# Kernel optimization log

Measured on AMD Instinct MI355X. Metric: run time of the kernel, lower is better.

## Reference

```python
import jax, jax.numpy as jnp
import numpy as np

D, S, L, W, H, V = 64, 64, 64, 300, 300, 50000
NEG = jnp.float32(-9999999.0)


def setup_inputs() -> dict:
    key = jax.random.key(0)
    ks = jax.random.split(key, 16)
    n = lambda k, shape, s=0.05: jax.random.normal(k, shape, dtype=jnp.float32) * s
    return {
        "word_indices": jax.random.randint(ks[0], (D, S, L), 0, V),
        "E": n(ks[1], (V, W), 0.1),
        "W_sent": n(ks[2], (H, W)), "b_sent": jnp.zeros((H,), jnp.float32),
        "W_par": n(ks[3], (H, H)), "b_par": jnp.zeros((H,), jnp.float32),
        "W_ch": n(ks[4], (H, H)), "b_ch": jnp.zeros((H,), jnp.float32),
        "w_root": n(ks[5], (H,)), "b_root": jnp.zeros((), jnp.float32),
        "root_embed": n(ks[6], (H,)),
        "W_r": n(ks[7], (H, 3 * H)), "b_r": jnp.zeros((H,), jnp.float32),
        "W_cls": n(ks[8], (2, H)), "b_cls": jnp.zeros((2,), jnp.float32),
    }


def reference(word_indices, E, W_sent, b_sent, W_par, b_par, W_ch, b_ch,
              w_root, b_root, root_embed, W_r, b_r, W_cls, b_cls):
    lrelu = lambda x: jax.nn.leaky_relu(x, 0.01)
    # Ragged pad+gather stage of the original, dense here (all lengths == L)
    word_embed = E[word_indices]                 # [D,S,L,W]
    # 0.5*(X[l-1] + reverse(reverse(X))[l-1]) == X[l-1]; LSTM outputs unused in source
    x_last = word_embed[:, :, -1, :]             # [D,S,W]
    enc = lrelu(x_last @ W_sent.T + b_sent)      # [D,S,H] sentence encodings
    # Pairwise parent-child edge scores (O(S^2) dots in the original loops)
    P = lrelu(enc @ W_par.T + b_par)             # [D,S,H]
    C = lrelu(enc @ W_ch.T + b_ch)               # [D,S,H]
    A = jnp.einsum('dih,djh->dij', P, C)         # [D,S,S]
    A = jnp.where(jnp.eye(S, dtype=bool)[None], NEG, A)
    A = jax.nn.softmax(A, axis=1)                # Softmax(dim=0) per doc: over parents i
    scores = enc @ w_root + b_root               # [D,S] root scores
    fri = jax.nn.softmax(scores, axis=1)         # Softmax(dim=0) over sentences
    # ri[i] = r_embeds([enc_i, sum_k A[k,i]*enc_k + fri_i*root, enc_i*sum_k A[i,k]])
    tmp = jnp.einsum('dki,dkh->dih', A, enc)     # [D,S,H]
    agg = tmp + fri[..., None] * root_embed      # [D,S,H]
    tmp3 = enc * A.sum(axis=2, keepdims=True)    # [D,S,H]
    ri = lrelu(jnp.concatenate([enc, agg, tmp3], axis=-1) @ W_r.T + b_r)  # [D,S,H]
    final = ri.mean(axis=1)                      # [D,H]
    out = final @ W_cls.T + b_cls                # [D,2]
    return out, A, fri
```

## Files before the change

kernel.cpp:

```cpp
#include <hip/hip_runtime.h>

#define NEG_INF (-9999999.0f)

typedef __attribute__((ext_vector_type(8))) short bf16x8;
typedef __attribute__((ext_vector_type(4))) float f32x4;
typedef unsigned short us;
typedef unsigned int u32;

#define MFMA16 __builtin_amdgcn_mfma_f32_16x16x32_bf16

__device__ __forceinline__ float b2f(us u) {
  union { unsigned int i; float f; } x; x.i = ((unsigned int)u) << 16; return x.f;
}
__device__ __forceinline__ us f2b(float f) {
  union { float f; unsigned int i; } x; x.f = f;
  unsigned int r = x.i + 0x7fffu + ((x.i >> 16) & 1u);
  return (us)(r >> 16);
}
__device__ __forceinline__ float lrelu(float v) { return v > 0.f ? v : 0.01f * v; }
__device__ __forceinline__ bf16x8 ld8(const us* p) { return *reinterpret_cast<const bf16x8*>(p); }
__device__ __forceinline__ int swz(int row) { return (row & 7) << 4; }

__global__ __launch_bounds__(256) void k_prep(
    const float* __restrict__ Ws, const float* __restrict__ Wp, const float* __restrict__ Wc,
    const float* __restrict__ Wr, const float* __restrict__ root,
    us* __restrict__ Wsb, us* __restrict__ Wpb, us* __restrict__ Wcb,
    us* __restrict__ Wr3b, float* __restrict__ c2) {
  int task = blockIdx.y;
  int gid = blockIdx.x * 256 + threadIdx.x;
  const int stride = 80 * 256;
  if (task < 3) {
    const float* src = (task == 0) ? Ws : (task == 1) ? Wp : Wc;
    us* dst = (task == 0) ? Wsb : (task == 1) ? Wpb : Wcb;
    for (int i = gid; i < 320 * 320; i += stride) {
      int r = i / 320, c = i - r * 320;
      dst[i] = (r < 300 && c < 300) ? f2b(src[r * 300 + c]) : (us)0;
    }
  } else if (task == 3) {
    for (int i = gid; i < 3 * 320 * 320; i += stride) {
      int seg = i / 102400, rem = i - seg * 102400;
      int r = rem / 320, c = rem - r * 320;
      Wr3b[i] = (r < 300 && c < 300) ? f2b(Wr[r * 900 + seg * 300 + c]) : (us)0;
    }
  } else {
    for (int i = gid; i < 320 * 8; i += stride) {
      int c = i >> 3, p = i & 7;
      float s = 0.f;
      if (c < 300)
        for (int h = p; h < 300; h += 8) s = fmaf(Wr[c * 900 + 300 + h], root[h], s);
      s += __shfl_xor(s, 1); s += __shfl_xor(s, 2); s += __shfl_xor(s, 4);
      if (p == 0) c2[c] = s;
    }
  }
}

template<int NT, int KS>
__device__ __forceinline__ void sweep2(const us* __restrict__ Alds, int r0, int r1, int q, int lo,
    const us* __restrict__ Bg, int n0, f32x4 (&acc)[2][NT]) {
  const char* ab = (const char*)Alds;
  const int a0o = r0 * 640, s0 = swz(r0);
  const int a1o = r1 * 640, s1 = swz(r1);
  const us* br[NT];
#pragma unroll
  for (int t = 0; t < NT; ++t)
    br[t] = Bg + (long)((n0 + t) * 16 + lo) * 320 + 8 * q;
  bf16x8 aC[2], aN[2], b0[NT], b1[NT];
  aC[0] = *(const bf16x8*)(ab + a0o + ((16 * q) ^ s0));
  aC[1] = *(const bf16x8*)(ab + a1o + ((16 * q) ^ s1));
  aN[0] = *(const bf16x8*)(ab + a0o + ((64 + 16 * q) ^ s0));
  aN[1] = *(const bf16x8*)(ab + a1o + ((64 + 16 * q) ^ s1));
#pragma unroll
  for (int t = 0; t < NT; ++t) b0[t] = ld8(br[t]);
#pragma unroll
  for (int t = 0; t < NT; ++t) b1[t] = ld8(br[t] + 32);
#pragma unroll
  for (int ks = 0; ks < KS - 2; ++ks) {
    bf16x8 aF[2], bF[NT];
    const int kb = 64 * (ks + 2) + 16 * q;
    aF[0] = *(const bf16x8*)(ab + a0o + (kb ^ s0));
    aF[1] = *(const bf16x8*)(ab + a1o + (kb ^ s1));
#pragma unroll
    for (int t = 0; t < NT; ++t) bF[t] = ld8(br[t] + (ks + 2) * 32);
#pragma unroll
    for (int t = 0; t < NT; ++t) {
      acc[0][t] = MFMA16(aC[0], b0[t], acc[0][t], 0, 0, 0);
      acc[1][t] = MFMA16(aC[1], b0[t], acc[1][t], 0, 0, 0);
    }
    aC[0] = aN[0]; aC[1] = aN[1]; aN[0] = aF[0]; aN[1] = aF[1];
#pragma unroll
    for (int t = 0; t < NT; ++t) { b0[t] = b1[t]; b1[t] = bF[t]; }
  }
#pragma unroll
  for (int t = 0; t < NT; ++t) {
    acc[0][t] = MFMA16(aC[0], b0[t], acc[0][t], 0, 0, 0);
    acc[1][t] = MFMA16(aC[1], b0[t], acc[1][t], 0, 0, 0);
  }
#pragma unroll
  for (int t = 0; t < NT; ++t) {
    acc[0][t] = MFMA16(aN[0], b1[t], acc[0][t], 0, 0, 0);
    acc[1][t] = MFMA16(aN[1], b1[t], acc[1][t], 0, 0, 0);
  }
}

__device__ __forceinline__ void epi_lds(const f32x4 (&acc)[2][5], const float* __restrict__ bias,
    us* __restrict__ dst, int mh, int nq, int lo, int q) {
#pragma unroll
  for (int mi = 0; mi < 2; ++mi)
#pragma unroll
    for (int tt = 0; tt < 5; ++tt) {
      int col = (nq * 5 + tt) * 16 + lo;
      if (col < 300) {
        float bb = bias[col];
#pragma unroll
        for (int r = 0; r < 4; ++r) {
          int row = (mh * 2 + mi) * 16 + 4 * q + r;
          *(us*)((char*)dst + row * 640 + ((2 * col) ^ swz(row))) =
              f2b(lrelu(acc[mi][tt][r] + bb));
        }
      }
    }
}

__global__ __launch_bounds__(512, 2) void k_mega(
    const int* __restrict__ wi, const float* __restrict__ E,
    const us* __restrict__ Wsb, const us* __restrict__ Wpb, const us* __restrict__ Wcb,
    const us* __restrict__ Wrb, const float* __restrict__ c2,
    const float* __restrict__ b_sent, const float* __restrict__ b_par,
    const float* __restrict__ b_ch,
    const float* __restrict__ w_root, const float* __restrict__ b_root,
    const float* __restrict__ b_r, const float* __restrict__ W_cls,
    const float* __restrict__ b_cls,
    float* __restrict__ outp, float* __restrict__ outA, float* __restrict__ outF) {
  __shared__ __align__(16) us BIG[61440];
  __shared__ __align__(16) float LA[64 * 68];
  __shared__ __align__(16) us AtL[64 * 72];
  __shared__ float pm[512], ps[512];
  __shared__ float scS[64], friS[64], rsS[64];
  __shared__ float finP[640];

  const int d = blockIdx.x, t = threadIdx.x;
  const int w = t >> 6, lane = t & 63, lo = lane & 15, q = lane >> 4;
  const int mh = w & 1, nq = w >> 1;
  const int r0 = mh * 32 + lo, r1 = r0 + 16;
  const f32x4 z4 = {0.f, 0.f, 0.f, 0.f};
  us* const Pl = BIG + 20480;
  us* const Cl = BIG + 40960;
  us* const G2T = BIG + 20480;

  {
    u32* zb = (u32*)BIG;
#pragma unroll
    for (int i = 0; i < 60; ++i) zb[t + i * 512] = 0u;
  }
  __syncthreads();

  {
    int s = t >> 3, p = t & 7;
    int widx = wi[((d * 64 + s) << 6) + 63];
    const float4* er = (const float4*)(E + (long)widx * 300);
    char* rowb = (char*)BIG + s * 640;
    int sw = swz(s);
    for (int j = p; j < 75; j += 8) {
      float4 v = er[j];
      ushort4 h4 = make_ushort4(f2b(v.x), f2b(v.y), f2b(v.z), f2b(v.w));
      *(ushort4*)(rowb + ((8 * j) ^ sw)) = h4;
    }
  }
  __syncthreads();

  {
    f32x4 acc[2][5];
#pragma unroll
    for (int a = 0; a < 2; ++a)
#pragma unroll
      for (int b = 0; b < 5; ++b) acc[a][b] = z4;
    sweep2<5, 10>(BIG, r0, r1, q, lo, Wsb, nq * 5, acc);
    __syncthreads();
    epi_lds(acc, b_sent, BIG, mh, nq, lo, q);
  }
  __syncthreads();

  {
    int i = t >> 3, p = t & 7;
    float s = 0.f;
    for (int cch = p; cch < 38; cch += 8) {
      bf16x8 v = *(const bf16x8*)((const char*)BIG + i * 640 + ((16 * cch) ^ swz(i)));
#pragma unroll
      for (int e = 0; e < 8; ++e) {
        int h = cch * 8 + e;
        if (h < 300) s = fmaf(b2f((us)v[e]), w_root[h], s);
      }
    }
    s += __shfl_xor(s, 1); s += __shfl_xor(s, 2); s += __shfl_xor(s, 4);
    if (p == 0) scS[i] = s + b_root[0];
  }
  __syncthreads();
  if (t < 64) {
    float sc = scS[t], m = sc;
#pragma unroll
    for (int o = 32; o > 0; o >>= 1) m = fmaxf(m, __shfl_xor(m, o));
    float e = expf(sc - m), sum = e;
#pragma unroll
    for (int o = 32; o > 0; o >>= 1) sum += __shfl_xor(sum, o);
    float f = e / sum;
    friS[t] = f;
    outF[d * 64 + t] = f;
  }

  {
    f32x4 acc[2][5];
#pragma unroll
    for (int a = 0; a < 2; ++a)
#pragma unroll
      for (int b = 0; b < 5; ++b) acc[a][b] = z4;
    sweep2<5, 10>(BIG, r0, r1, q, lo, Wpb, nq * 5, acc);
    epi_lds(acc, b_par, Pl, mh, nq, lo, q);
  }
  {
    f32x4 acc[2][5];
#pragma unroll
    for (int a = 0; a < 2; ++a)
#pragma unroll
      for (int b = 0; b < 5; ++b) acc[a][b] = z4;
    sweep2<5, 10>(BIG, r0, r1, q, lo, Wcb, nq * 5, acc);
    epi_lds(acc, b_ch, Cl, mh, nq, lo, q);
  }
  __syncthreads();

  {
    int m = w >> 1, np = (w & 1) * 2;
    int arow = m * 16 + lo;
    int brow0 = np * 16 + lo, brow1 = brow0 + 16;
    int sa = swz(arow), sb0 = swz(brow0), sb1 = swz(brow1);
    f32x4 a0 = z4, a1 = z4;
#pragma unroll
    for (int ks = 0; ks < 10; ++ks) {
      int kb = 64 * ks + 16 * q;
      bf16x8 av  = *(const bf16x8*)((const char*)Pl + arow * 640 + (kb ^ sa));
      bf16x8 bv0 = *(const bf16x8*)((const char*)Cl + brow0 * 640 + (kb ^ sb0));
      bf16x8 bv1 = *(const bf16x8*)((const char*)Cl + brow1 * 640 + (kb ^ sb1));
      a0 = MFMA16(av, bv0, a0, 0, 0, 0);
      a1 = MFMA16(av, bv1, a1, 0, 0, 0);
    }
#pragma unroll
    for (int r = 0; r < 4; ++r) {
      int row = m * 16 + 4 * q + r;
      int c0 = np * 16 + lo, c1 = c0 + 16;
      LA[row * 68 + c0] = (row == c0) ? NEG_INF : a0[r];
      LA[row * 68 + c1] = (row == c1) ? NEG_INF : a1[r];
    }
  }
  __syncthreads();

  {
    int j = lane, p2 = w;
    float mx = -3.0e38f;
#pragma unroll
    for (int ii = 0; ii < 8; ++ii) mx = fmaxf(mx, LA[(p2 * 8 + ii) * 68 + j]);
    pm[p2 * 64 + j] = mx;
    __syncthreads();
    float gm = pm[j];
#pragma unroll
    for (int k = 1; k < 8; ++k) gm = fmaxf(gm, pm[k * 64 + j]);
    float ev[8], s = 0.f;
#pragma unroll
    for (int ii = 0; ii < 8; ++ii) {
      float e = expf(LA[(p2 * 8 + ii) * 68 + j] - gm);
      ev[ii] = e; s += e;
    }
    ps[p2 * 64 + j] = s;
    __syncthreads();
    float tot = ps[j];
#pragma unroll
    for (int k = 1; k < 8; ++k) tot += ps[k * 64 + j];
    float inv = 1.f / tot;
    float* Ad = outA + (long)d * 4096;
#pragma unroll
    for (int ii = 0; ii < 8; ++ii) {
      int i = p2 * 8 + ii;
      float a = ev[ii] * inv;
      Ad[i * 64 + j] = a;
      AtL[j * 72 + i] = f2b(a);
      LA[i * 68 + j] = a;
    }
  }
  __syncthreads();
  if (t < 64) {
    float s = 0.f;
    for (int jj = 0; jj < 64; ++jj) s += LA[t * 68 + jj];
    rsS[t] = s;
  }

  {
    f32x4 acc[2][5];
#pragma unroll
    for (int a = 0; a < 2; ++a)
#pragma unroll
      for (int b = 0; b < 5; ++b) acc[a][b] = z4;
    sweep2<5, 10>(BIG, r0, r1, q, lo, Wrb + 102400, nq * 5, acc);
#pragma unroll
    for (int mi = 0; mi < 2; ++mi)
#pragma unroll
      for (int tt = 0; tt < 5; ++tt) {
        int col = (nq * 5 + tt) * 16 + lo;
        if (col < 300) {
#pragma unroll
          for (int r = 0; r < 4; ++r) {
            int row = (mh * 2 + mi) * 16 + 4 * q + r;
            G2T[col * 72 + row] = f2b(acc[mi][tt][r]);
          }
        }
      }
    for (int i2 = t; i2 < 720; i2 += 512) ((u32*)(G2T + 21600))[i2] = 0u;
  }
  __syncthreads();

  {
    f32x4 am[2][5], ag[2][5];
#pragma unroll
    for (int a = 0; a < 2; ++a)
#pragma unroll
      for (int b = 0; b < 5; ++b) { am[a][b] = z4; ag[a][b] = z4; }
    sweep2<5, 10>(BIG, r0, r1, q, lo, Wrb, nq * 5, am);
    sweep2<5, 10>(BIG, r0, r1, q, lo, Wrb + 204800, nq * 5, ag);
#pragma unroll
    for (int ks = 0; ks < 2; ++ks) {
      bf16x8 aA = *(const bf16x8*)(AtL + r0 * 72 + 32 * ks + 8 * q);
      bf16x8 aB = *(const bf16x8*)(AtL + r1 * 72 + 32 * ks + 8 * q);
#pragma unroll
      for (int tt = 0; tt < 5; ++tt) {
        bf16x8 bv = *(const bf16x8*)(G2T + ((nq * 5 + tt) * 16 + lo) * 72 + 32 * ks + 8 * q);
        am[0][tt] = MFMA16(aA, bv, am[0][tt], 0, 0, 0);
        am[1][tt] = MFMA16(aB, bv, am[1][tt], 0, 0, 0);
      }
    }
#pragma unroll
    for (int tt = 0; tt < 5; ++tt) {
      int col = (nq * 5 + tt) * 16 + lo;
      float bb = (col < 300) ? b_r[col] : 0.f;
      float cc = c2[col];
      float csum = 0.f;
#pragma unroll
      for (int mi = 0; mi < 2; ++mi)
#pragma unroll
        for (int r = 0; r < 4; ++r) {
          int i = (mh * 2 + mi) * 16 + 4 * q + r;
          csum += lrelu(am[mi][tt][r] + rsS[i] * ag[mi][tt][r] + friS[i] * cc + bb);
        }
      csum += __shfl_xor(csum, 16);
      csum += __shfl_xor(csum, 32);
      if (q == 0) finP[mh * 320 + col] = csum;
    }
  }
  __syncthreads();

  if (t < 128) {
    int cls = t >> 6, ln = t & 63;
    float s = 0.f;
    for (int h = ln; h < 300; h += 64)
      s += (finP[h] + finP[320 + h]) * W_cls[cls * 300 + h];
#pragma unroll
    for (int o = 32; o > 0; o >>= 1) s += __shfl_xor(s, o);
    if (ln == 0) outp[d * 2 + cls] = s * 0.015625f + b_cls[cls];
  }
}

extern "C" void kernel_launch(void* const* d_in, const int* in_sizes, int n_in,
                              void* d_out, int out_size, void* d_ws, size_t ws_size,
                              hipStream_t stream) {
  const int*   wi     = (const int*)d_in[0];
  const float* E      = (const float*)d_in[1];
  const float* W_sent = (const float*)d_in[2];
  const float* b_sent = (const float*)d_in[3];
  const float* W_par  = (const float*)d_in[4];
  const float* b_par  = (const float*)d_in[5];
  const float* W_ch   = (const float*)d_in[6];
  const float* b_ch   = (const float*)d_in[7];
  const float* w_root = (const float*)d_in[8];
  const float* b_root = (const float*)d_in[9];
  const float* root_e = (const float*)d_in[10];
  const float* W_r    = (const float*)d_in[11];
  const float* b_r    = (const float*)d_in[12];
  const float* W_cls  = (const float*)d_in[13];
  const float* b_cls  = (const float*)d_in[14];

  us* B = (us*)d_ws;
  us* Wsb  = B;
  us* Wpb  = B + 102400;
  us* Wcb  = B + 204800;
  us* Wr3b = B + 307200;
  float* c2 = (float*)(B + 614400);

  float* outp = (float*)d_out;
  float* outA = outp + 128;
  float* outF = outp + 128 + 262144;

  k_prep<<<dim3(80, 5), 256, 0, stream>>>(W_sent, W_par, W_ch, W_r, root_e,
                                          Wsb, Wpb, Wcb, Wr3b, c2);
  k_mega<<<64, 512, 0, stream>>>(wi, E, Wsb, Wpb, Wcb, Wr3b, c2,
                                 b_sent, b_par, b_ch, w_root, b_root,
                                 b_r, W_cls, b_cls, outp, outA, outF);
}
```

Baseline: 211.9 us.

## Double mega-kernel block to 1024 threads and overlap independent GEMM stages

The per-document kernel now runs 16 waves instead of 8. Each wave covers 16 rows for the sentence and final GEMMs. The parent and child projections run concurrently on separate wave halves, and the A-independent G2 GEMM overlaps with the attention-score and softmax stage. The rowsum-scaled term is folded into the accumulator before the Wr sweep, which removes one accumulator set. Zeroing now covers only the padding columns, and the prep kernel uses more blocks. The change aims to raise the limited parallelism from 64 blocks, at the cost of higher per-thread register pressure limits and more divergent control flow.

```diff
diff --git a/kernel.cpp b/kernel.cpp
--- a/kernel.cpp
+++ b/kernel.cpp
@@ -28,7 +28,7 @@
     us* __restrict__ Wr3b, float* __restrict__ c2) {
   int task = blockIdx.y;
   int gid = blockIdx.x * 256 + threadIdx.x;
-  const int stride = 80 * 256;
+  const int stride = 240 * 256;
   if (task < 3) {
     const float* src = (task == 0) ? Ws : (task == 1) ? Wp : Wc;
     us* dst = (task == 0) ? Wsb : (task == 1) ? Wpb : Wcb;
@@ -54,52 +54,53 @@
   }
 }
 
-template<int NT, int KS>
-__device__ __forceinline__ void sweep2(const us* __restrict__ Alds, int r0, int r1, int q, int lo,
-    const us* __restrict__ Bg, int n0, f32x4 (&acc)[2][NT]) {
+template<int M, int NT, int KS>
+__device__ __forceinline__ void sweepM(const us* __restrict__ Alds, const int (&rr)[M],
+    int q, int lo, const us* __restrict__ Bg, int n0, f32x4 (&acc)[M][NT]) {
   const char* ab = (const char*)Alds;
-  const int a0o = r0 * 640, s0 = swz(r0);
-  const int a1o = r1 * 640, s1 = swz(r1);
+  int ao[M], sw[M];
+#pragma unroll
+  for (int m = 0; m < M; ++m) { ao[m] = rr[m] * 640; sw[m] = swz(rr[m]); }
   const us* br[NT];
 #pragma unroll
   for (int t = 0; t < NT; ++t)
     br[t] = Bg + (long)((n0 + t) * 16 + lo) * 320 + 8 * q;
-  bf16x8 aC[2], aN[2], b0[NT], b1[NT];
-  aC[0] = *(const bf16x8*)(ab + a0o + ((16 * q) ^ s0));
-  aC[1] = *(const bf16x8*)(ab + a1o + ((16 * q) ^ s1));
-  aN[0] = *(const bf16x8*)(ab + a0o + ((64 + 16 * q) ^ s0));
-  aN[1] = *(const bf16x8*)(ab + a1o + ((64 + 16 * q) ^ s1));
+  bf16x8 aC[M], aN[M], b0[NT], b1[NT];
+#pragma unroll
+  for (int m = 0; m < M; ++m) {
+    aC[m] = *(const bf16x8*)(ab + ao[m] + ((16 * q) ^ sw[m]));
+    aN[m] = *(const bf16x8*)(ab + ao[m] + ((64 + 16 * q) ^ sw[m]));
+  }
 #pragma unroll
   for (int t = 0; t < NT; ++t) b0[t] = ld8(br[t]);
 #pragma unroll
   for (int t = 0; t < NT; ++t) b1[t] = ld8(br[t] + 32);
 #pragma unroll
   for (int ks = 0; ks < KS - 2; ++ks) {
-    bf16x8 aF[2], bF[NT];
+    bf16x8 aF[M], bF[NT];
     const int kb = 64 * (ks + 2) + 16 * q;
-    aF[0] = *(const bf16x8*)(ab + a0o + (kb ^ s0));
-    aF[1] = *(const bf16x8*)(ab + a1o + (kb ^ s1));
+#pragma unroll
+    for (int m = 0; m < M; ++m) aF[m] = *(const bf16x8*)(ab + ao[m] + (kb ^ sw[m]));
 #pragma unroll
     for (int t = 0; t < NT; ++t) bF[t] = ld8(br[t] + (ks + 2) * 32);
 #pragma unroll
-    for (int t = 0; t < NT; ++t) {
-      acc[0][t] = MFMA16(aC[0], b0[t], acc[0][t], 0, 0, 0);
-      acc[1][t] = MFMA16(aC[1], b0[t], acc[1][t], 0, 0, 0);
-    }
-    aC[0] = aN[0]; aC[1] = aN[1]; aN[0] = aF[0]; aN[1] = aF[1];
+    for (int t = 0; t < NT; ++t)
+#pragma unroll
+      for (int m = 0; m < M; ++m)
+        acc[m][t] = MFMA16(aC[m], b0[t], acc[m][t], 0, 0, 0);
+#pragma unroll
+    for (int m = 0; m < M; ++m) { aC[m] = aN[m]; aN[m] = aF[m]; }
 #pragma unroll
     for (int t = 0; t < NT; ++t) { b0[t] = b1[t]; b1[t] = bF[t]; }
   }
 #pragma unroll
-  for (int t = 0; t < NT; ++t) {
-    acc[0][t] = MFMA16(aC[0], b0[t], acc[0][t], 0, 0, 0);
-    acc[1][t] = MFMA16(aC[1], b0[t], acc[1][t], 0, 0, 0);
-  }
-#pragma unroll
-  for (int t = 0; t < NT; ++t) {
-    acc[0][t] = MFMA16(aN[0], b1[t], acc[0][t], 0, 0, 0);
-    acc[1][t] = MFMA16(aN[1], b1[t], acc[1][t], 0, 0, 0);
-  }
+  for (int t = 0; t < NT; ++t)
+#pragma unroll
+    for (int m = 0; m < M; ++m) acc[m][t] = MFMA16(aC[m], b0[t], acc[m][t], 0, 0, 0);
+#pragma unroll
+  for (int t = 0; t < NT; ++t)
+#pragma unroll
+    for (int m = 0; m < M; ++m) acc[m][t] = MFMA16(aN[m], b1[t], acc[m][t], 0, 0, 0);
 }
 
 __device__ __forceinline__ void epi_lds(const f32x4 (&acc)[2][5], const float* __restrict__ bias,
@@ -121,7 +122,24 @@
     }
 }
 
-__global__ __launch_bounds__(512, 2) void k_mega(
+__device__ __forceinline__ void epi1(const f32x4 (&acc)[5], const float* __restrict__ bias,
+    us* __restrict__ dst, int mg, int nq, int lo, int q) {
+#pragma unroll
+  for (int tt = 0; tt < 5; ++tt) {
+    int col = (nq * 5 + tt) * 16 + lo;
+    if (col < 300) {
+      float bb = bias[col];
+#pragma unroll
+      for (int r = 0; r < 4; ++r) {
+        int row = mg * 16 + 4 * q + r;
+        *(us*)((char*)dst + row * 640 + ((2 * col) ^ swz(row))) =
+            f2b(lrelu(acc[tt][r] + bb));
+      }
+    }
+  }
+}
+
+__global__ __launch_bounds__(1024) void k_mega(
     const int* __restrict__ wi, const float* __restrict__ E,
     const us* __restrict__ Wsb, const us* __restrict__ Wpb, const us* __restrict__ Wcb,
     const us* __restrict__ Wrb, const float* __restrict__ c2,
@@ -136,54 +154,51 @@
   __shared__ __align__(16) us AtL[64 * 72];
   __shared__ float pm[512], ps[512];
   __shared__ float scS[64], friS[64], rsS[64];
-  __shared__ float finP[640];
+  __shared__ float finP2[4 * 320];
 
   const int d = blockIdx.x, t = threadIdx.x;
   const int w = t >> 6, lane = t & 63, lo = lane & 15, q = lane >> 4;
-  const int mh = w & 1, nq = w >> 1;
-  const int r0 = mh * 32 + lo, r1 = r0 + 16;
+  const int mg = w & 3, nq = w >> 2;
   const f32x4 z4 = {0.f, 0.f, 0.f, 0.f};
   us* const Pl = BIG + 20480;
   us* const Cl = BIG + 40960;
   us* const G2T = BIG + 20480;
 
-  {
-    u32* zb = (u32*)BIG;
-#pragma unroll
-    for (int i = 0; i < 60; ++i) zb[t + i * 512] = 0u;
-  }
-  __syncthreads();
-
-  {
-    int s = t >> 3, p = t & 7;
+  for (int i = t; i < 6144; i += 1024) {
+    int p = i >> 11, rem = i & 2047, r = rem >> 5, wd = rem & 31;
+    *(u32*)((char*)BIG + p * 40960 + r * 640 + 512 + wd * 4) = 0u;
+  }
+  __syncthreads();
+
+  {
+    int s = t >> 4, p = t & 15;
     int widx = wi[((d * 64 + s) << 6) + 63];
     const float4* er = (const float4*)(E + (long)widx * 300);
     char* rowb = (char*)BIG + s * 640;
     int sw = swz(s);
-    for (int j = p; j < 75; j += 8) {
+    for (int j = p; j < 75; j += 16) {
       float4 v = er[j];
-      ushort4 h4 = make_ushort4(f2b(v.x), f2b(v.y), f2b(v.z), f2b(v.w));
-      *(ushort4*)(rowb + ((8 * j) ^ sw)) = h4;
-    }
-  }
-  __syncthreads();
-
-  {
-    f32x4 acc[2][5];
-#pragma unroll
-    for (int a = 0; a < 2; ++a)
-#pragma unroll
-      for (int b = 0; b < 5; ++b) acc[a][b] = z4;
-    sweep2<5, 10>(BIG, r0, r1, q, lo, Wsb, nq * 5, acc);
+      *(ushort4*)(rowb + ((8 * j) ^ sw)) =
+          make_ushort4(f2b(v.x), f2b(v.y), f2b(v.z), f2b(v.w));
+    }
+  }
+  __syncthreads();
+
+  {
+    int rr[1] = { mg * 16 + lo };
+    f32x4 acc[1][5];
+#pragma unroll
+    for (int b = 0; b < 5; ++b) acc[0][b] = z4;
+    sweepM<1, 5, 10>(BIG, rr, q, lo, Wsb, nq * 5, acc);
     __syncthreads();
-    epi_lds(acc, b_sent, BIG, mh, nq, lo, q);
-  }
-  __syncthreads();
-
-  {
-    int i = t >> 3, p = t & 7;
+    epi1(acc[0], b_sent, BIG, mg, nq, lo, q);
+  }
+  __syncthreads();
+
+  {
+    int i = t >> 4, p = t & 15;
     float s = 0.f;
-    for (int cch = p; cch < 38; cch += 8) {
+    for (int cch = p; cch < 38; cch += 16) {
       bf16x8 v = *(const bf16x8*)((const char*)BIG + i * 640 + ((16 * cch) ^ swz(i)));
 #pragma unroll
       for (int e = 0; e < 8; ++e) {
@@ -191,10 +206,26 @@
         if (h < 300) s = fmaf(b2f((us)v[e]), w_root[h], s);
       }
     }
-    s += __shfl_xor(s, 1); s += __shfl_xor(s, 2); s += __shfl_xor(s, 4);
+    s += __shfl_xor(s, 1); s += __shfl_xor(s, 2); s += __shfl_xor(s, 4); s += __shfl_xor(s, 8);
     if (p == 0) scS[i] = s + b_root[0];
   }
-  __syncthreads();
+
+  {
+    int w2 = w & 7, mh = w2 & 1, nqq = w2 >> 1;
+    int rr[2] = { mh * 32 + lo, mh * 32 + 16 + lo };
+    const us* Bg = (w < 8) ? Wpb : Wcb;
+    const float* bias = (w < 8) ? b_par : b_ch;
+    us* dst = (w < 8) ? Pl : Cl;
+    f32x4 acc[2][5];
+#pragma unroll
+    for (int a = 0; a < 2; ++a)
+#pragma unroll
+      for (int b = 0; b < 5; ++b) acc[a][b] = z4;
+    sweepM<2, 5, 10>(BIG, rr, q, lo, Bg, nqq * 5, acc);
+    epi_lds(acc, bias, dst, mh, nqq, lo, q);
+  }
+  __syncthreads();
+
   if (t < 64) {
     float sc = scS[t], m = sc;
 #pragma unroll
@@ -207,27 +238,8 @@
     outF[d * 64 + t] = f;
   }
 
-  {
-    f32x4 acc[2][5];
-#pragma unroll
-    for (int a = 0; a < 2; ++a)
-#pragma unroll
-      for (int b = 0; b < 5; ++b) acc[a][b] = z4;
-    sweep2<5, 10>(BIG, r0, r1, q, lo, Wpb, nq * 5, acc);
-    epi_lds(acc, b_par, Pl, mh, nq, lo, q);
-  }
-  {
-    f32x4 acc[2][5];
-#pragma unroll
-    for (int a = 0; a < 2; ++a)
-#pragma unroll
-      for (int b = 0; b < 5; ++b) acc[a][b] = z4;
-    sweep2<5, 10>(BIG, r0, r1, q, lo, Wcb, nq * 5, acc);
-    epi_lds(acc, b_ch, Cl, mh, nq, lo, q);
-  }
-  __syncthreads();
-
-  {
+  f32x4 g2acc[2][5];
+  if (w < 8) {
     int m = w >> 1, np = (w & 1) * 2;
     int arow = m * 16 + lo;
     int brow0 = np * 16 + lo, brow1 = brow0 + 16;
@@ -249,39 +261,70 @@
       LA[row * 68 + c0] = (row == c0) ? NEG_INF : a0[r];
       LA[row * 68 + c1] = (row == c1) ? NEG_INF : a1[r];
     }
+  } else {
+    int w2 = w - 8, mh = w2 & 1, nqq = w2 >> 1;
+    int rr[2] = { mh * 32 + lo, mh * 32 + 16 + lo };
+#pragma unroll
+    for (int a = 0; a < 2; ++a)
+#pragma unroll
+      for (int b = 0; b < 5; ++b) g2acc[a][b] = z4;
+    sweepM<2, 5, 10>(BIG, rr, q, lo, Wrb + 102400, nqq * 5, g2acc);
   }
   __syncthreads();
 
   {
     int j = lane, p2 = w;
-    float mx = -3.0e38f;
-#pragma unroll
-    for (int ii = 0; ii < 8; ++ii) mx = fmaxf(mx, LA[(p2 * 8 + ii) * 68 + j]);
-    pm[p2 * 64 + j] = mx;
+    float ev[8], gm = 0.f;
+    if (w < 8) {
+      float mx = -3.0e38f;
+#pragma unroll
+      for (int ii = 0; ii < 8; ++ii) mx = fmaxf(mx, LA[(p2 * 8 + ii) * 68 + j]);
+      pm[p2 * 64 + j] = mx;
+    } else {
+      int w2 = w - 8, mh = w2 & 1, nqq = w2 >> 1;
+#pragma unroll
+      for (int mi = 0; mi < 2; ++mi)
+#pragma unroll
+        for (int tt = 0; tt < 5; ++tt) {
+          int col = (nqq * 5 + tt) * 16 + lo;
+          if (col < 300)
+#pragma unroll
+            for (int r = 0; r < 4; ++r) {
+              int row = (mh * 2 + mi) * 16 + 4 * q + r;
+              G2T[col * 72 + row] = f2b(g2acc[mi][tt][r]);
+            }
+        }
+      for (int i2 = t - 512; i2 < 720; i2 += 512)
+        ((u32*)(G2T + 21600))[i2] = 0u;
+    }
     __syncthreads();
-    float gm = pm[j];
-#pragma unroll
-    for (int k = 1; k < 8; ++k) gm = fmaxf(gm, pm[k * 64 + j]);
-    float ev[8], s = 0.f;
-#pragma unroll
-    for (int ii = 0; ii < 8; ++ii) {
-      float e = expf(LA[(p2 * 8 + ii) * 68 + j] - gm);
-      ev[ii] = e; s += e;
-    }
-    ps[p2 * 64 + j] = s;
+    float ssum = 0.f;
+    if (w < 8) {
+      gm = pm[j];
+#pragma unroll
+      for (int k = 1; k < 8; ++k) gm = fmaxf(gm, pm[k * 64 + j]);
+#pragma unroll
+      for (int ii = 0; ii < 8; ++ii) {
+        float e = expf(LA[(p2 * 8 + ii) * 68 + j] - gm);
+        ev[ii] = e; ssum += e;
+      }
+      ps[p2 * 64 + j] = ssum;
+    }
     __syncthreads();
-    float tot = ps[j];
-#pragma unroll
-    for (int k = 1; k < 8; ++k) tot += ps[k * 64 + j];
-    float inv = 1.f / tot;
-    float* Ad = outA + (long)d * 4096;
-#pragma unroll
-    for (int ii = 0; ii < 8; ++ii) {
-      int i = p2 * 8 + ii;
-      float a = ev[ii] * inv;
-      Ad[i * 64 + j] = a;
-      AtL[j * 72 + i] = f2b(a);
-      LA[i * 68 + j] = a;
+    if (w < 8) {
+      float tot = ps[j];
+#pragma unroll
+      for (int k = 1; k < 8; ++k) tot += ps[k * 64 + j];
+      float inv = 1.f / tot;
+      float* Ad = outA + (long)d * 4096;
+#pragma unroll
+      for (int ii = 0; ii < 8; ++ii) {
+        int i = p2 * 8 + ii;
+        float a = ev[ii] * inv;
+        Ad[i * 64 + j] = a;
+        AtL[j * 72 + i] = f2b(a);
+        LA[i * 68 + j] = a;
+      }
     }
   }
   __syncthreads();
@@ -290,48 +333,27 @@
     for (int jj = 0; jj < 64; ++jj) s += LA[t * 68 + jj];
     rsS[t] = s;
   }
-
-  {
-    f32x4 acc[2][5];
-#pragma unroll
-    for (int a = 0; a < 2; ++a)
-#pragma unroll
-      for (int b = 0; b < 5; ++b) acc[a][b] = z4;
-    sweep2<5, 10>(BIG, r0, r1, q, lo, Wrb + 102400, nq * 5, acc);
-#pragma unroll
-    for (int mi = 0; mi < 2; ++mi)
-#pragma unroll
-      for (int tt = 0; tt < 5; ++tt) {
-        int col = (nq * 5 + tt) * 16 + lo;
-        if (col < 300) {
-#pragma unroll
-          for (int r = 0; r < 4; ++r) {
-            int row = (mh * 2 + mi) * 16 + 4 * q + r;
-            G2T[col * 72 + row] = f2b(acc[mi][tt][r]);
-          }
-        }
-      }
-    for (int i2 = t; i2 < 720; i2 += 512) ((u32*)(G2T + 21600))[i2] = 0u;
-  }
-  __syncthreads();
-
-  {
-    f32x4 am[2][5], ag[2][5];
-#pragma unroll
-    for (int a = 0; a < 2; ++a)
-#pragma unroll
-      for (int b = 0; b < 5; ++b) { am[a][b] = z4; ag[a][b] = z4; }
-    sweep2<5, 10>(BIG, r0, r1, q, lo, Wrb, nq * 5, am);
-    sweep2<5, 10>(BIG, r0, r1, q, lo, Wrb + 204800, nq * 5, ag);
+  __syncthreads();
+
+  {
+    int rr[1] = { mg * 16 + lo };
+    f32x4 am[1][5];
+#pragma unroll
+    for (int b = 0; b < 5; ++b) am[0][b] = z4;
+    sweepM<1, 5, 10>(BIG, rr, q, lo, Wrb + 204800, nq * 5, am);
+#pragma unroll
+    for (int tt = 0; tt < 5; ++tt)
+#pragma unroll
+      for (int r = 0; r < 4; ++r)
+        am[0][tt][r] *= rsS[mg * 16 + 4 * q + r];
+    sweepM<1, 5, 10>(BIG, rr, q, lo, Wrb, nq * 5, am);
 #pragma unroll
     for (int ks = 0; ks < 2; ++ks) {
-      bf16x8 aA = *(const bf16x8*)(AtL + r0 * 72 + 32 * ks + 8 * q);
-      bf16x8 aB = *(const bf16x8*)(AtL + r1 * 72 + 32 * ks + 8 * q);
+      bf16x8 aA = *(const bf16x8*)(AtL + (mg * 16 + lo) * 72 + 32 * ks + 8 * q);
 #pragma unroll
       for (int tt = 0; tt < 5; ++tt) {
         bf16x8 bv = *(const bf16x8*)(G2T + ((nq * 5 + tt) * 16 + lo) * 72 + 32 * ks + 8 * q);
         am[0][tt] = MFMA16(aA, bv, am[0][tt], 0, 0, 0);
-        am[1][tt] = MFMA16(aB, bv, am[1][tt], 0, 0, 0);
       }
     }
 #pragma unroll
@@ -341,15 +363,13 @@
       float cc = c2[col];
       float csum = 0.f;
 #pragma unroll
-      for (int mi = 0; mi < 2; ++mi)
-#pragma unroll
-        for (int r = 0; r < 4; ++r) {
-          int i = (mh * 2 + mi) * 16 + 4 * q + r;
-          csum += lrelu(am[mi][tt][r] + rsS[i] * ag[mi][tt][r] + friS[i] * cc + bb);
-        }
+      for (int r = 0; r < 4; ++r) {
+        int i = mg * 16 + 4 * q + r;
+        csum += lrelu(am[0][tt][r] + friS[i] * cc + bb);
+      }
       csum += __shfl_xor(csum, 16);
       csum += __shfl_xor(csum, 32);
-      if (q == 0) finP[mh * 320 + col] = csum;
+      if (q == 0) finP2[mg * 320 + col] = csum;
     }
   }
   __syncthreads();
@@ -358,7 +378,8 @@
     int cls = t >> 6, ln = t & 63;
     float s = 0.f;
     for (int h = ln; h < 300; h += 64)
-      s += (finP[h] + finP[320 + h]) * W_cls[cls * 300 + h];
+      s += (finP2[h] + finP2[320 + h] + finP2[640 + h] + finP2[960 + h]) *
+           W_cls[cls * 300 + h];
 #pragma unroll
     for (int o = 32; o > 0; o >>= 1) s += __shfl_xor(s, o);
     if (ln == 0) outp[d * 2 + cls] = s * 0.015625f + b_cls[cls];
@@ -395,9 +416,9 @@
   float* outA = outp + 128;
   float* outF = outp + 128 + 262144;
 
-  k_prep<<<dim3(80, 5), 256, 0, stream>>>(W_sent, W_par, W_ch, W_r, root_e,
-                                          Wsb, Wpb, Wcb, Wr3b, c2);
-  k_mega<<<64, 512, 0, stream>>>(wi, E, Wsb, Wpb, Wcb, Wr3b, c2,
-                                 b_sent, b_par, b_ch, w_root, b_root,
-                                 b_r, W_cls, b_cls, outp, outA, outF);
-}
+  k_prep<<<dim3(240, 5), 256, 0, stream>>>(W_sent, W_par, W_ch, W_r, root_e,
+                                           Wsb, Wpb, Wcb, Wr3b, c2);
+  k_mega<<<64, 1024, 0, stream>>>(wi, E, Wsb, Wpb, Wcb, Wr3b, c2,
+                                  b_sent, b_par, b_ch, w_root, b_root,
+                                  b_r, W_cls, b_cls, outp, outA, outF);
+}
```

New measurement: 252.7 us. 1.19x slower.
